# Kernel tuning notes

Hardware: AMD Instinct MI355X
Metric: run time of the kernel (lower is better)

The kernel has to match this reference:

```python
import jax, jax.numpy as jnp
import numpy as np
import math

B, S, DM, H, N_HASHES, BUCKET = 1, 1024, 512, 8, 8, 64
HD = DM // H
N_BUCKETS = max(2, 2 * (S // (2 * BUCKET)))   # 16
ROT = max(1, N_BUCKETS // 2)                  # 8


def setup_inputs() -> dict:
    key = jax.random.key(0)
    ks = jax.random.split(key, 6)
    sc = 1.0 / math.sqrt(DM)
    return {
        "x": jax.random.normal(ks[0], (B, S, DM), dtype=jnp.float32),
        "w_qk": (jax.random.normal(ks[1], (DM, DM), dtype=jnp.float32) * sc),
        "b_qk": jnp.zeros((DM,), dtype=jnp.float32),
        "w_v": (jax.random.normal(ks[2], (DM, DM), dtype=jnp.float32) * sc),
        "b_v": jnp.zeros((DM,), dtype=jnp.float32),
        "w_o": (jax.random.normal(ks[3], (DM, DM), dtype=jnp.float32) * sc),
        "b_o": jnp.zeros((DM,), dtype=jnp.float32),
        # random rotations used for LSH hashing (torch.randn in hash_vectors)
        "rotations": jax.random.normal(ks[4], (N_HASHES, H, HD, ROT), dtype=jnp.float32),
    }


def reference(x, w_qk, b_qk, w_v, b_v, w_o, b_o, rotations):
    # projections, split heads: (B, H, S, HD)
    qk = (x @ w_qk + b_qk).reshape(B, S, H, HD).transpose(0, 2, 1, 3)
    v = (x @ w_v + b_v).reshape(B, S, H, HD).transpose(0, 2, 1, 3)

    # LSH bucket assignment: (B, H, S, n_hashes)
    rot = jnp.einsum('bhnd,rhdc->bhnrc', qk, rotations)
    rot = jnp.concatenate([rot, -rot], axis=-1)
    buckets = jnp.argmax(rot, axis=-1)

    # The original gathers (batch, head, pos) jointly per bucket, so attention
    # mixes across batch and head; flatten exactly the same way.
    N = B * H * S
    qkf = qk.reshape(N, HD)
    vf = v.reshape(N, HD)
    bkf = buckets.reshape(N, N_HASHES).T  # (n_hashes, N)

    # dots are shared across hash rounds; only the bucket mask changes
    dots = (qkf @ qkf.T) / math.sqrt(HD)  # (N, N)

    def body(acc, bk):
        same = bk[:, None] == bk[None, :]  # bucket-equality mask
        w = jax.nn.softmax(jnp.where(same, dots, -jnp.inf), axis=-1)
        return acc + w @ vf, None

    out, _ = jax.lax.scan(body, jnp.zeros_like(vf), bkf)
    out = out / N_HASHES

    out = out.reshape(B, H, S, HD).transpose(0, 2, 1, 3).reshape(B, S, DM)
    return out @ w_o + b_o
```

## Files before the change

### kernel.cpp

```cpp
#include <hip/hip_runtime.h>
#include <math.h>

#define S 1024
#define DM 512
#define H 8
#define HD 64
#define NH 8
#define NB 16
#define N 8192
#define SCALE 0.125f
#define EXP2C 0.18033688f

typedef __attribute__((ext_vector_type(4))) float f32x4;
typedef __attribute__((ext_vector_type(8))) short s16x8;
typedef __attribute__((ext_vector_type(4))) short s16x4;

__device__ __forceinline__ short f2bf(float f) {
  union { float f; unsigned u; } a; a.f = f;
  unsigned r = a.u + 0x7fffu + ((a.u >> 16) & 1u);
  return (short)(r >> 16);
}
__device__ __forceinline__ float bf2f(short h) {
  union { unsigned u; float f; } a; a.u = ((unsigned)(unsigned short)h) << 16;
  return a.f;
}
__device__ __forceinline__ int f2bf2(float lo, float hi) {
  return (int)(unsigned short)f2bf(lo) | (((int)f2bf(hi)) << 16);
}

#if __has_builtin(__builtin_amdgcn_mfma_f32_16x16x16_bf16)
#define MFMA_PV(a, b, c) __builtin_amdgcn_mfma_f32_16x16x16_bf16(a, b, c, 0, 0, 0)
#else
#define MFMA_PV(a, b, c) __builtin_amdgcn_mfma_f32_16x16x16bf16_1k(a, b, c, 0, 0, 0)
#endif

__global__ __launch_bounds__(256) void wprep_kernel(
    const float* __restrict__ wqk, const float* __restrict__ wv,
    const float* __restrict__ wo, const float* __restrict__ x,
    short* __restrict__ wtqk, short* __restrict__ wtv, short* __restrict__ wto,
    short* __restrict__ xs, int* __restrict__ cz) {
  int tid = threadIdx.x;
  if (blockIdx.x == 0) cz[tid] = 0;
  if (blockIdx.x >= 192) {
    int xb = blockIdx.x - 192;
    size_t base = ((size_t)xb * 256 + tid) * 16;
    const float4* xp = (const float4*)(x + base);
    float4 f0 = xp[0], f1 = xp[1], f2 = xp[2], f3 = xp[3];
    float vv[16] = {f0.x,f0.y,f0.z,f0.w, f1.x,f1.y,f1.z,f1.w,
                    f2.x,f2.y,f2.z,f2.w, f3.x,f3.y,f3.z,f3.w};
    s16x8 h0[2], h1[2], h2[2];
#pragma unroll
    for (int g = 0; g < 2; ++g)
#pragma unroll
      for (int i = 0; i < 8; ++i) {
        float v = vv[g * 8 + i];
        short a = f2bf(v); float r1 = v - bf2f(a);
        short b = f2bf(r1); short c = f2bf(r1 - bf2f(b));
        h0[g][i] = a; h1[g][i] = b; h2[g][i] = c;
      }
    s16x8* p0 = (s16x8*)(xs + base);
    s16x8* p1 = (s16x8*)(xs + (size_t)S * DM + base);
    s16x8* p2 = (s16x8*)(xs + (size_t)2 * S * DM + base);
    p0[0] = h0[0]; p0[1] = h0[1];
    p1[0] = h1[0]; p1[1] = h1[1];
    p2[0] = h2[0]; p2[1] = h2[1];
    return;
  }
  int mat = blockIdx.x >> 6;
  int tile = blockIdx.x & 63;
  int kt = tile >> 3, dt = tile & 7;
  const float* w = (mat == 0) ? wqk : ((mat == 1) ? wv : wo);

  __shared__ float wlds[64 * 68];
  int kr = tid >> 2, c4 = tid & 3;
  const float4* src = (const float4*)(w + (size_t)(kt * 64 + kr) * DM + dt * 64 + c4 * 16);
#pragma unroll
  for (int i = 0; i < 4; ++i) {
    float4 v = src[i];
    float* d = &wlds[kr * 68 + c4 * 16 + i * 4];
    d[0] = v.x; d[1] = v.y; d[2] = v.z; d[3] = v.w;
  }
  __syncthreads();
  int dr = tid >> 2, kc = tid & 3;
  s16x8 h0a, h0b, h1a, h1b, h2a, h2b;
#pragma unroll
  for (int i = 0; i < 8; ++i) {
    float v = wlds[(kc * 16 + i) * 68 + dr];
    short a = f2bf(v); float r1 = v - bf2f(a);
    short b = f2bf(r1); short c = f2bf(r1 - bf2f(b));
    h0a[i] = a; h1a[i] = b; h2a[i] = c;
  }
#pragma unroll
  for (int i = 0; i < 8; ++i) {
    float v = wlds[(kc * 16 + 8 + i) * 68 + dr];
    short a = f2bf(v); float r1 = v - bf2f(a);
    short b = f2bf(r1); short c = f2bf(r1 - bf2f(b));
    h0b[i] = a; h1b[i] = b; h2b[i] = c;
  }
  size_t dst = (size_t)(dt * 64 + dr) * DM + kt * 64 + kc * 16;
  if (mat == 0) {
    s16x8* p0 = (s16x8*)(wtqk + dst);
    s16x8* p1 = (s16x8*)(wtqk + (size_t)DM * DM + dst);
    s16x8* p2 = (s16x8*)(wtqk + (size_t)2 * DM * DM + dst);
    p0[0] = h0a; p0[1] = h0b; p1[0] = h1a; p1[1] = h1b; p2[0] = h2a; p2[1] = h2b;
  } else if (mat == 1) {
    s16x8* p = (s16x8*)(wtv + dst); p[0] = h0a; p[1] = h0b;
  } else {
    s16x8* p = (s16x8*)(wto + dst); p[0] = h0a; p[1] = h0b;
  }
}

#define PST 72
__global__ __launch_bounds__(256) void projmm_kernel(
    const short* __restrict__ xs, const short* __restrict__ wtqk,
    const short* __restrict__ wtv,
    const float* __restrict__ bqk, const float* __restrict__ bv,
    float* __restrict__ qkpart, short* __restrict__ vb) {
  int mt = blockIdx.x & 15;
  int rest = blockIdx.x >> 4;
  int sp = rest >> 3;
  int head = rest & 7;
  bool isv = (sp == 6);
  int xl = isv ? 0 : ((0x210100 >> (sp << 2)) & 0xF);
  int wl = isv ? 0 : ((0x012010 >> (sp << 2)) & 0xF);
  const short* wt = isv ? wtv : (wtqk + (size_t)wl * DM * DM);
  const short* xsl = xs + (size_t)xl * S * DM;

  __shared__ short a_lds[2][64 * PST];
  __shared__ short b_lds[2][64 * PST];

  int tid = threadIdx.x;
  int wave = tid >> 6, lane = tid & 63;
  int col = lane & 15, quad = lane >> 4;
  int mh = wave & 1, nh2 = wave >> 1;

  f32x4 acc[2][2];
#pragma unroll
  for (int i = 0; i < 2; ++i)
#pragma unroll
    for (int j = 0; j < 2; ++j) acc[i][j] = (f32x4){0.f, 0.f, 0.f, 0.f};

  int sr = tid >> 2, c4 = tid & 3;
  int gran = sr * PST + ((c4 ^ (sr & 3)) << 4);

  {
    const s16x8* xp = (const s16x8*)(xsl + (size_t)(mt * 64 + sr) * DM + c4 * 16);
    s16x8* ad = (s16x8*)&a_lds[0][gran];
    ad[0] = xp[0]; ad[1] = xp[1];
    const s16x8* wp = (const s16x8*)(wt + (size_t)(head * 64 + sr) * DM + c4 * 16);
    s16x8* bd = (s16x8*)&b_lds[0][gran];
    bd[0] = wp[0]; bd[1] = wp[1];
  }
  __syncthreads();

  for (int ci = 0; ci < 8; ++ci) {
    int cur = ci & 1, nxt = cur ^ 1;
    s16x8 px0, px1, pw0, pw1;
    bool has = (ci + 1) < 8;
    if (has) {
      int kc = ci + 1;
      const s16x8* xp = (const s16x8*)(xsl + (size_t)(mt * 64 + sr) * DM + kc * 64 + c4 * 16);
      px0 = xp[0]; px1 = xp[1];
      const s16x8* wp = (const s16x8*)(wt + (size_t)(head * 64 + sr) * DM + kc * 64 + c4 * 16);
      pw0 = wp[0]; pw1 = wp[1];
    }
#pragma unroll
    for (int s2 = 0; s2 < 2; ++s2) {
      s16x8 af[2], bfv[2];
#pragma unroll
      for (int mi = 0; mi < 2; ++mi) {
        int row = mh * 32 + mi * 16 + col;
        int cidx = ((s2 << 1) + (quad >> 1)) ^ (row & 3);
        af[mi] = *(const s16x8*)&a_lds[cur][row * PST + (cidx << 4) + ((quad & 1) << 3)];
      }
#pragma unroll
      for (int ni = 0; ni < 2; ++ni) {
        int row = nh2 * 32 + ni * 16 + col;
        int cidx = ((s2 << 1) + (quad >> 1)) ^ (row & 3);
        bfv[ni] = *(const s16x8*)&b_lds[cur][row * PST + (cidx << 4) + ((quad & 1) << 3)];
      }
#pragma unroll
      for (int mi = 0; mi < 2; ++mi)
#pragma unroll
        for (int ni = 0; ni < 2; ++ni)
          acc[mi][ni] = __builtin_amdgcn_mfma_f32_16x16x32_bf16(af[mi], bfv[ni],
                                                               acc[mi][ni], 0, 0, 0);
    }
    if (has) {
      s16x8* ad = (s16x8*)&a_lds[nxt][gran];
      ad[0] = px0; ad[1] = px1;
      s16x8* bd = (s16x8*)&b_lds[nxt][gran];
      bd[0] = pw0; bd[1] = pw1;
    }
    __syncthreads();
  }
  if (isv) {
#pragma unroll
    for (int ni = 0; ni < 2; ++ni) {
      int nl = nh2 * 32 + ni * 16 + col;
      float bb = bv[head * 64 + nl];
#pragma unroll
      for (int mi = 0; mi < 2; ++mi)
#pragma unroll
        for (int u = 0; u < 4; ++u) {
          int s = mt * 64 + mh * 32 + mi * 16 + quad * 4 + u;
          vb[((size_t)head * S + s) * HD + nl] = f2bf(acc[mi][ni][u] + bb);
        }
    }
  } else {
    float* dst = qkpart + (size_t)sp * N * HD;
#pragma unroll
    for (int ni = 0; ni < 2; ++ni) {
      int nl = nh2 * 32 + ni * 16 + col;
      float bb = (sp == 0) ? bqk[head * 64 + nl] : 0.f;
#pragma unroll
      for (int mi = 0; mi < 2; ++mi)
#pragma unroll
        for (int u = 0; u < 4; ++u) {
          int s = mt * 64 + mh * 32 + mi * 16 + quad * 4 + u;
          dst[((size_t)head * S + s) * HD + nl] = acc[mi][ni][u] + bb;
        }
    }
  }
}

__global__ __launch_bounds__(256) void sumslab_kernel(
    const float* __restrict__ qkpart, float* __restrict__ qkf,
    short* __restrict__ qkb) {
  int idx = blockIdx.x * 256 + threadIdx.x;
  f32x4 s = ((const f32x4*)qkpart)[idx];
#pragma unroll
  for (int sl = 1; sl < 6; ++sl)
    s += ((const f32x4*)(qkpart + (size_t)sl * N * HD))[idx];
  ((f32x4*)qkf)[idx] = s;
  int2 pk = make_int2(f2bf2(s[0], s[1]), f2bf2(s[2], s[3]));
  *(int2*)(qkb + (size_t)idx * 4) = pk;
}

__global__ __launch_bounds__(256) void bucket_kernel(
    const float* __restrict__ qkf, const float* __restrict__ rot,
    int* __restrict__ cursor, int* __restrict__ perm2) {
  __shared__ float Rl[HD * 8];
  __shared__ int lcnt[NB];
  __shared__ int gbase[NB];
  int tid = threadIdx.x;
  int g = blockIdx.x * 256 + tid;
  int n = g & (N - 1);
  int r = g >> 13;
  int h = n >> 10;
  const float* R = rot + (size_t)((r * H + h) * HD) * 8;
  if (tid < 128) ((f32x4*)Rl)[tid] = ((const f32x4*)R)[tid];
  if (tid < NB) lcnt[tid] = 0;

  f32x4 qv[16];
  const f32x4* q4 = (const f32x4*)(qkf + (size_t)n * HD);
#pragma unroll
  for (int d4 = 0; d4 < 16; ++d4) qv[d4] = q4[d4];
  __syncthreads();

  float v[8];
#pragma unroll
  for (int c = 0; c < 8; ++c) v[c] = 0.f;
#pragma unroll
  for (int d4 = 0; d4 < 16; ++d4) {
    f32x4 q = qv[d4];
#pragma unroll
    for (int j = 0; j < 4; ++j) {
      const f32x4* Rr = (const f32x4*)&Rl[(d4 * 4 + j) * 8];
      f32x4 r0 = Rr[0], r1 = Rr[1];
      float qj = q[j];
#pragma unroll
      for (int c = 0; c < 4; ++c) v[c] = fmaf(qj, r0[c], v[c]);
#pragma unroll
      for (int c = 0; c < 4; ++c) v[4 + c] = fmaf(qj, r1[c], v[4 + c]);
    }
  }
  float best = v[0];
  int bi = 0;
#pragma unroll
  for (int c = 1; c < 16; ++c) {
    float val = (c < 8) ? v[c] : -v[c - 8];
    if (val > best) { best = val; bi = c; }
  }

  int lrank = atomicAdd(&lcnt[bi], 1);
  __syncthreads();
  if (tid < NB) gbase[tid] = atomicAdd(&cursor[(r << 4) + tid], lcnt[tid]);
  __syncthreads();
  perm2[(((size_t)(r << 4) + bi) << 13) + gbase[bi] + lrank] = n;
}

#define KT 64
#define KST 72
#define VTS2 72
#define VBUF (64 * VTS2)
__global__ __launch_bounds__(512) void attn_kernel(
    const short* __restrict__ qkb, const short* __restrict__ vb,
    const int* __restrict__ perm2, const int* __restrict__ cursor,
    short* __restrict__ accumB) {
  int bx = blockIdx.x;
  int rb = bx & 127;
  int chunk = bx >> 7;
  int r = rb >> 4;
  int cnt = cursor[rb];
  int q0 = chunk << 7;
  if (q0 >= cnt) return;
  const int* plist = perm2 + ((size_t)rb << 13);

  int tid = threadIdx.x;
  int wave = tid >> 6, lane = tid & 63;
  int col = lane & 15, quad = lane >> 4;

  __shared__ short k_lds[2][KT * KST];
  __shared__ short v_lds[2][VBUF];

  int qslot = q0 + (wave << 4) + col;
  bool qvalid = qslot < cnt;
  int qidx = plist[qvalid ? qslot : 0];
  bool wactive = (q0 + (wave << 4)) < cnt;

  for (int e = tid; e < VBUF; e += 512) ((int*)v_lds)[e] = 0;

  s16x8 qa[2];
#pragma unroll
  for (int s2 = 0; s2 < 2; ++s2)
    qa[s2] = *(const s16x8*)(qkb + (size_t)qidx * HD + s2 * 32 + quad * 8);
  __syncthreads();

  float lsum = 0.f;
  f32x4 o0 = {0,0,0,0}, o1 = {0,0,0,0}, o2 = {0,0,0,0}, o3 = {0,0,0,0};

  int jsk = tid >> 2, csk = tid & 3;
  bool stager = tid < 256;
  int kgran = jsk * KST + ((csk ^ (jsk & 3)) << 4);
  int ksw0 = (jsk + 16 * csk) & 63;
  int ksw1 = (jsk + 16 * csk + 4) & 63;
  int vdr = csk * 16 * VTS2;

  int vrow = col * VTS2;
  int vco = (col >> 3) << 2;

  {
    int nj = min(KT, cnt);
    if (stager && jsk < nj) {
      int gk = plist[jsk];
      const s16x8* kp = (const s16x8*)(qkb + (size_t)gk * HD + (csk << 4));
      const s16x8* vp = (const s16x8*)(vb + (size_t)gk * HD + (csk << 4));
      s16x8 a0 = kp[0], a1 = kp[1], b0 = vp[0], b1 = vp[1];
      s16x8* kd = (s16x8*)&k_lds[0][kgran];
      kd[0] = a0; kd[1] = a1;
      short* vt = &v_lds[0][vdr];
#pragma unroll
      for (int i = 0; i < 8; ++i) {
        vt[i * VTS2 + ksw0] = b0[i];
        vt[(8 + i) * VTS2 + ksw1] = b1[i];
      }
    }
  }
  int pln = 0; bool pln_ok = false;
  if (stager) {
    int i1 = KT + jsk;
    pln_ok = i1 < cnt;
    pln = plist[i1 < 8192 ? i1 : 8191];
  }
  __syncthreads();

  int ntiles = (cnt + KT - 1) >> 6;
  for (int t = 0; t < ntiles; ++t) {
    int jt = t << 6;
    int cur = t & 1, nxt = cur ^ 1;
    s16x8 a0, a1, b0, b1;
    bool pf_ok = stager && pln_ok;
    if (pf_ok) {
      const s16x8* kp = (const s16x8*)(qkb + (size_t)pln * HD + (csk << 4));
      const s16x8* vp = (const s16x8*)(vb + (size_t)pln * HD + (csk << 4));
      a0 = kp[0]; a1 = kp[1]; b0 = vp[0]; b1 = vp[1];
    }
    int pl2 = 0; bool pl2_ok = false;
    if (stager) {
      int i2 = jt + 2 * KT + jsk;
      pl2_ok = i2 < cnt;
      pl2 = plist[i2 < 8192 ? i2 : 8191];
    }
    if (wactive) {
      const short* vtc = v_lds[cur];
      const short* ktc = k_lds[cur];
      f32x4 sA = {0,0,0,0}, sB = {0,0,0,0}, sC = {0,0,0,0}, sD = {0,0,0,0};
#define QK1(C, SA) { int key = ((C) << 4) + col; \
      const short* kb = &ktc[key * KST]; \
      { int cidx = (quad >> 1) ^ (key & 3); \
        s16x8 kf = *(const s16x8*)&kb[(cidx << 4) + ((quad & 1) << 3)]; \
        SA = __builtin_amdgcn_mfma_f32_16x16x32_bf16(kf, qa[0], SA, 0, 0, 0); } \
      { int cidx = (2 + (quad >> 1)) ^ (key & 3); \
        s16x8 kf = *(const s16x8*)&kb[(cidx << 4) + ((quad & 1) << 3)]; \
        SA = __builtin_amdgcn_mfma_f32_16x16x32_bf16(kf, qa[1], SA, 0, 0, 0); } }
      __builtin_amdgcn_s_setprio(1);
      QK1(0, sA) QK1(1, sB) QK1(2, sC) QK1(3, sD)
      __builtin_amdgcn_s_setprio(0);
      s16x4 p0, p1, p2, p3;
#define SM1(C, SA, PF) { int kbase = jt + ((C) << 4) + (quad << 2); \
      float pw[4]; \
      if (kbase + 4 <= cnt) { \
        _Pragma("unroll") for (int u = 0; u < 4; ++u) pw[u] = exp2f(SA[u] * EXP2C); \
      } else { \
        _Pragma("unroll") for (int u = 0; u < 4; ++u) \
          pw[u] = (kbase + u < cnt) ? exp2f(SA[u] * EXP2C) : 0.f; \
      } \
      lsum += (pw[0] + pw[1]) + (pw[2] + pw[3]); \
      int dA_, dB_; \
      asm("v_cvt_pk_bf16_f32 %0, %1, %2" : "=v"(dA_) : "v"(pw[0]), "v"(pw[1])); \
      asm("v_cvt_pk_bf16_f32 %0, %1, %2" : "=v"(dB_) : "v"(pw[2]), "v"(pw[3])); \
      ((int*)&PF)[0] = dA_; ((int*)&PF)[1] = dB_; }
      SM1(0, sA, p0) SM1(1, sB, p1) SM1(2, sC, p2) SM1(3, sD, p3)
#define PV1(C, PF) { int k0s = ((C) << 4) + (quad << 2) + vco; \
      s16x4 va = *(const s16x4*)&vtc[vrow + (k0s & 63)]; \
      s16x4 vb_ = *(const s16x4*)&vtc[16 * VTS2 + vrow + ((k0s + 16) & 63)]; \
      s16x4 vc = *(const s16x4*)&vtc[32 * VTS2 + vrow + ((k0s + 32) & 63)]; \
      s16x4 vd = *(const s16x4*)&vtc[48 * VTS2 + vrow + ((k0s + 48) & 63)]; \
      o0 = MFMA_PV(PF, va, o0); o1 = MFMA_PV(PF, vb_, o1); \
      o2 = MFMA_PV(PF, vc, o2); o3 = MFMA_PV(PF, vd, o3); }
      __builtin_amdgcn_s_setprio(1);
      PV1(0, p0) PV1(1, p1) PV1(2, p2) PV1(3, p3)
      __builtin_amdgcn_s_setprio(0);
#undef QK1
#undef SM1
#undef PV1
    }
    if (pf_ok) {
      s16x8* kd = (s16x8*)&k_lds[nxt][kgran];
      kd[0] = a0; kd[1] = a1;
      short* vt = &v_lds[nxt][vdr];
#pragma unroll
      for (int i = 0; i < 8; ++i) {
        vt[i * VTS2 + ksw0] = b0[i];
        vt[(8 + i) * VTS2 + ksw1] = b1[i];
      }
    }
    pln = pl2; pln_ok = pl2_ok;
    __syncthreads();
  }

  lsum += __shfl_xor(lsum, 16);
  lsum += __shfl_xor(lsum, 32);
  float inv = 1.f / lsum;
#pragma unroll
  for (int u = 0; u < 4; ++u) {
    int slot = (quad << 2) + u;
    int spos = q0 + (wave << 4) + slot;
    float inv_u = __shfl(inv, slot);
    int qidx_u = __shfl(qidx, slot);
    if (spos < cnt) {
      short* dst = accumB + ((size_t)r * N + qidx_u) * HD + col;
      dst[0]  = f2bf(o0[u] * inv_u);
      dst[16] = f2bf(o1[u] * inv_u);
      dst[32] = f2bf(o2[u] * inv_u);
      dst[48] = f2bf(o3[u] * inv_u);
    }
  }
}

__global__ __launch_bounds__(256) void asum_kernel(
    const short* __restrict__ accumB, short* __restrict__ asumB) {
  size_t idx = (size_t)blockIdx.x * 256 + threadIdx.x;
  float a[8];
#pragma unroll
  for (int i = 0; i < 8; ++i) a[i] = 0.f;
#pragma unroll
  for (int r = 0; r < NH; ++r) {
    s16x8 h = *(const s16x8*)(accumB + (size_t)r * N * HD + idx * 8);
#pragma unroll
    for (int i = 0; i < 8; ++i) a[i] += bf2f(h[i]);
  }
  s16x8 o;
#pragma unroll
  for (int i = 0; i < 8; ++i) o[i] = f2bf(a[i] * 0.125f);
  *(s16x8*)(asumB + idx * 8) = o;
}

__global__ __launch_bounds__(256) void outproj_kernel(
    const short* __restrict__ asumB, const short* __restrict__ wto,
    const float* __restrict__ bo, float* __restrict__ out) {
  int mt = blockIdx.x & 31;
  int nt = blockIdx.x >> 5;
  __shared__ short a_lds[2][32 * PST];
  __shared__ short b_lds[2][64 * PST];
  int tid = threadIdx.x;
  int wave = tid >> 6, lane = tid & 63;
  int col = lane & 15, quad = lane >> 4;
  int mi2 = wave & 1, nh2 = wave >> 1;

  f32x4 acc[2];
  acc[0] = (f32x4){0.f,0.f,0.f,0.f};
  acc[1] = (f32x4){0.f,0.f,0.f,0.f};

  bool isA = tid < 128;
  int sr = tid >> 2, c4 = tid & 3;
  int agran = sr * PST + ((c4 ^ (sr & 3)) << 4);
  int dl = (tid - 128) >> 1, gp = tid & 1;

  {
    if (isA) {
      const s16x8* ap = (const s16x8*)(asumB + ((size_t)0 * S + mt * 32 + sr) * HD + c4 * 16);
      s16x8* ad = (s16x8*)&a_lds[0][agran];
      ad[0] = ap[0]; ad[1] = ap[1];
    } else {
      const s16x8* wp = (const s16x8*)(wto + (size_t)(nt * 64 + dl) * DM + gp * 32);
      int g0 = gp * 2;
      s16x8* d0 = (s16x8*)&b_lds[0][dl * PST + ((g0 ^ (dl & 3)) << 4)];
      d0[0] = wp[0]; d0[1] = wp[1];
      s16x8* d1 = (s16x8*)&b_lds[0][dl * PST + (((g0 + 1) ^ (dl & 3)) << 4)];
      d1[0] = wp[2]; d1[1] = wp[3];
    }
  }
  __syncthreads();

  for (int kc = 0; kc < 8; ++kc) {
    int cur = kc & 1, nxt = cur ^ 1;
    bool has = kc + 1 < 8;
    s16x8 pa0, pa1, pb0, pb1, pb2, pb3;
    if (has) {
      if (isA) {
        const s16x8* ap = (const s16x8*)(asumB +
            ((size_t)(kc + 1) * S + mt * 32 + sr) * HD + c4 * 16);
        pa0 = ap[0]; pa1 = ap[1];
      } else {
        const s16x8* wp = (const s16x8*)(wto + (size_t)(nt * 64 + dl) * DM +
                                         (kc + 1) * 64 + gp * 32);
        pb0 = wp[0]; pb1 = wp[1]; pb2 = wp[2]; pb3 = wp[3];
      }
    }
#pragma unroll
    for (int s2 = 0; s2 < 2; ++s2) {
      int arow = mi2 * 16 + col;
      int acidx = ((s2 << 1) + (quad >> 1)) ^ (arow & 3);
      s16x8 af = *(const s16x8*)&a_lds[cur][arow * PST + (acidx << 4) + ((quad & 1) << 3)];
      s16x8 bfv[2];
#pragma unroll
      for (int ni = 0; ni < 2; ++ni) {
        int brow = nh2 * 32 + ni * 16 + col;
        int bcidx = ((s2 << 1) + (quad >> 1)) ^ (brow & 3);
        bfv[ni] = *(const s16x8*)&b_lds[cur][brow * PST + (bcidx << 4) + ((quad & 1) << 3)];
      }
#pragma unroll
      for (int ni = 0; ni < 2; ++ni)
        acc[ni] = __builtin_amdgcn_mfma_f32_16x16x32_bf16(af, bfv[ni], acc[ni], 0, 0, 0);
    }
    if (has) {
      if (isA) {
        s16x8* ad = (s16x8*)&a_lds[nxt][agran];
        ad[0] = pa0; ad[1] = pa1;
      } else {
        int g0 = gp * 2;
        s16x8* d0 = (s16x8*)&b_lds[nxt][dl * PST + ((g0 ^ (dl & 3)) << 4)];
        d0[0] = pb0; d0[1] = pb1;
        s16x8* d1 = (s16x8*)&b_lds[nxt][dl * PST + (((g0 + 1) ^ (dl & 3)) << 4)];
        d1[0] = pb2; d1[1] = pb3;
      }
    }
    __syncthreads();
  }
#pragma unroll
  for (int ni = 0; ni < 2; ++ni) {
    int nl = nh2 * 32 + ni * 16 + col;
    int dgl = nt * 64 + nl;
    float bb = bo[dgl];
#pragma unroll
    for (int u = 0; u < 4; ++u) {
      int s = mt * 32 + mi2 * 16 + quad * 4 + u;
      out[(size_t)s * DM + dgl] = acc[ni][u] + bb;
    }
  }
}

extern "C" void kernel_launch(void* const* d_in, const int* in_sizes, int n_in,
                              void* d_out, int out_size, void* d_ws, size_t ws_size,
                              hipStream_t stream) {
  const float* x    = (const float*)d_in[0];
  const float* w_qk = (const float*)d_in[1];
  const float* b_qk = (const float*)d_in[2];
  const float* w_v  = (const float*)d_in[3];
  const float* b_v  = (const float*)d_in[4];
  const float* w_o  = (const float*)d_in[5];
  const float* b_o  = (const float*)d_in[6];
  const float* rot  = (const float*)d_in[7];
  float* out = (float*)d_out;

  char* ws = (char*)d_ws;
  const size_t MB = 1024u * 1024u;
  short* qkb    = (short*)(ws);
  short* vb     = (short*)(ws + 1 * MB);
  float* qkpart = (float*)(ws + 2 * MB);
  short* accumB = (short*)(ws + 2 * MB);
  int* perm2    = (int*)(ws + 10 * MB);
  float* qkf    = (float*)(ws + 18 * MB);
  short* wtqk   = (short*)(ws + 20 * MB);
  short* wtv    = (short*)(ws + 20 * MB + 1536u * 1024);
  short* wto    = (short*)(ws + 22 * MB);
  int* cursor   = (int*)(ws + 22 * MB + 512u * 1024);
  short* xs     = (short*)(ws + 23 * MB);
  short* asumB  = (short*)(ws + 26 * MB);

  wprep_kernel<<<320, 256, 0, stream>>>(w_qk, w_v, w_o, x, wtqk, wtv, wto, xs, cursor);
  projmm_kernel<<<896, 256, 0, stream>>>(xs, wtqk, wtv, b_qk, b_v, qkpart, vb);
  sumslab_kernel<<<512, 256, 0, stream>>>(qkpart, qkf, qkb);
  bucket_kernel<<<(NH * N) / 256, 256, 0, stream>>>(qkf, rot, cursor, perm2);
  attn_kernel<<<16 * 128, 512, 0, stream>>>(qkb, vb, perm2, cursor, accumB);
  asum_kernel<<<256, 256, 0, stream>>>(accumB, asumB);
  outproj_kernel<<<256, 256, 0, stream>>>(asumB, wto, b_o, out);
}
```

Baseline: 136.1 us.

## Replace split-K partial slabs with atomic accumulation and drop sumslab kernel

The six split-K partial products for the QK projection are now added directly into a zeroed qkf buffer with float atomicAdd, instead of being written to separate slabs and summed by a dedicated kernel. The zeroing moves into the weight-prep kernel, and the bf16 conversion of qk moves into the bucket kernel (round 0 threads only). This removes one launch and the slab write/read traffic. In exchange it adds atomic contention and makes the fp32 summation order nondeterministic.

```diff
diff --git a/kernel.cpp b/kernel.cpp
--- a/kernel.cpp
+++ b/kernel.cpp
@@ -38,11 +38,17 @@
     const float* __restrict__ wqk, const float* __restrict__ wv,
     const float* __restrict__ wo, const float* __restrict__ x,
     short* __restrict__ wtqk, short* __restrict__ wtv, short* __restrict__ wto,
-    short* __restrict__ xs, int* __restrict__ cz) {
+    short* __restrict__ xs, float* __restrict__ qkf, int* __restrict__ cz) {
   int tid = threadIdx.x;
   if (blockIdx.x == 0) cz[tid] = 0;
   if (blockIdx.x >= 192) {
     int xb = blockIdx.x - 192;
+    {
+      f32x4* z = (f32x4*)(qkf + (size_t)xb * 4096);
+#pragma unroll
+      for (int i = 0; i < 4; ++i)
+        z[tid * 4 + i] = (f32x4){0.f, 0.f, 0.f, 0.f};
+    }
     size_t base = ((size_t)xb * 256 + tid) * 16;
     const float4* xp = (const float4*)(x + base);
     float4 f0 = xp[0], f1 = xp[1], f2 = xp[2], f3 = xp[3];
@@ -115,7 +121,7 @@
     const short* __restrict__ xs, const short* __restrict__ wtqk,
     const short* __restrict__ wtv,
     const float* __restrict__ bqk, const float* __restrict__ bv,
-    float* __restrict__ qkpart, short* __restrict__ vb) {
+    float* __restrict__ qkf, short* __restrict__ vb) {
   int mt = blockIdx.x & 15;
   int rest = blockIdx.x >> 4;
   int sp = rest >> 3;
@@ -208,7 +214,6 @@
         }
     }
   } else {
-    float* dst = qkpart + (size_t)sp * N * HD;
 #pragma unroll
     for (int ni = 0; ni < 2; ++ni) {
       int nl = nh2 * 32 + ni * 16 + col;
@@ -218,28 +223,16 @@
 #pragma unroll
         for (int u = 0; u < 4; ++u) {
           int s = mt * 64 + mh * 32 + mi * 16 + quad * 4 + u;
-          dst[((size_t)head * S + s) * HD + nl] = acc[mi][ni][u] + bb;
+          atomicAdd(&qkf[((size_t)head * S + s) * HD + nl], acc[mi][ni][u] + bb);
         }
     }
   }
-}
-
-__global__ __launch_bounds__(256) void sumslab_kernel(
-    const float* __restrict__ qkpart, float* __restrict__ qkf,
-    short* __restrict__ qkb) {
-  int idx = blockIdx.x * 256 + threadIdx.x;
-  f32x4 s = ((const f32x4*)qkpart)[idx];
-#pragma unroll
-  for (int sl = 1; sl < 6; ++sl)
-    s += ((const f32x4*)(qkpart + (size_t)sl * N * HD))[idx];
-  ((f32x4*)qkf)[idx] = s;
-  int2 pk = make_int2(f2bf2(s[0], s[1]), f2bf2(s[2], s[3]));
-  *(int2*)(qkb + (size_t)idx * 4) = pk;
 }
 
 __global__ __launch_bounds__(256) void bucket_kernel(
     const float* __restrict__ qkf, const float* __restrict__ rot,
-    int* __restrict__ cursor, int* __restrict__ perm2) {
+    int* __restrict__ cursor, int* __restrict__ perm2,
+    short* __restrict__ qkb) {
   __shared__ float Rl[HD * 8];
   __shared__ int lcnt[NB];
   __shared__ int gbase[NB];
@@ -257,6 +250,15 @@
 #pragma unroll
   for (int d4 = 0; d4 < 16; ++d4) qv[d4] = q4[d4];
   __syncthreads();
+
+  if (r == 0) {
+    int2* qb = (int2*)(qkb + (size_t)n * HD);
+#pragma unroll
+    for (int d4 = 0; d4 < 16; ++d4) {
+      f32x4 q = qv[d4];
+      qb[d4] = make_int2(f2bf2(q[0], q[1]), f2bf2(q[2], q[3]));
+    }
+  }
 
   float v[8];
 #pragma unroll
@@ -589,7 +591,6 @@
   const size_t MB = 1024u * 1024u;
   short* qkb    = (short*)(ws);
   short* vb     = (short*)(ws + 1 * MB);
-  float* qkpart = (float*)(ws + 2 * MB);
   short* accumB = (short*)(ws + 2 * MB);
   int* perm2    = (int*)(ws + 10 * MB);
   float* qkf    = (float*)(ws + 18 * MB);
@@ -600,10 +601,10 @@
   short* xs     = (short*)(ws + 23 * MB);
   short* asumB  = (short*)(ws + 26 * MB);
 
-  wprep_kernel<<<320, 256, 0, stream>>>(w_qk, w_v, w_o, x, wtqk, wtv, wto, xs, cursor);
-  projmm_kernel<<<896, 256, 0, stream>>>(xs, wtqk, wtv, b_qk, b_v, qkpart, vb);
-  sumslab_kernel<<<512, 256, 0, stream>>>(qkpart, qkf, qkb);
-  bucket_kernel<<<(NH * N) / 256, 256, 0, stream>>>(qkf, rot, cursor, perm2);
+  wprep_kernel<<<320, 256, 0, stream>>>(w_qk, w_v, w_o, x, wtqk, wtv, wto,
+                                        xs, qkf, cursor);
+  projmm_kernel<<<896, 256, 0, stream>>>(xs, wtqk, wtv, b_qk, b_v, qkf, vb);
+  bucket_kernel<<<(NH * N) / 256, 256, 0, stream>>>(qkf, rot, cursor, perm2, qkb);
   attn_kernel<<<16 * 128, 512, 0, stream>>>(qkb, vb, perm2, cursor, accumB);
   asum_kernel<<<256, 256, 0, stream>>>(accumB, asumB);
   outproj_kernel<<<256, 256, 0, stream>>>(asumB, wto, b_o, out);
```

New measurement: 138.4 us. Within noise of the previous version (+1.7%).
